# Performance work log

Measured on AMD Instinct MI355X. Metric: run time of the kernel, lower is better.

Reference implementation:

```python
import jax, jax.numpy as jnp
import numpy as np

EPS = 1e-5

def _bn_relu(y, mean, var, scale, bias):
    # y: (b, c, n); eval-mode batchnorm over channel axis, then ReLU
    inv = scale / jnp.sqrt(var + EPS)
    return jax.nn.relu((y - mean[None, :, None]) * inv[None, :, None] + bias[None, :, None])

def setup_inputs() -> dict:
    key = jax.random.key(0)
    ks = jax.random.split(key, 6)
    b, c, n, cr = 4, 256, 4096, 32
    inp = {
        'x': jax.random.normal(ks[0], (b, c, n), jnp.float32),
        'w_q': jax.random.normal(ks[1], (cr, c), jnp.float32) * (1.0 / np.sqrt(c)),
        'w_k': jax.random.normal(ks[2], (cr, c), jnp.float32) * (1.0 / np.sqrt(c)),
        'w_v': jax.random.normal(ks[3], (c, c), jnp.float32) * (1.0 / np.sqrt(c)),
        'bn1_scale': jnp.ones((cr,), jnp.float32), 'bn1_bias': jnp.zeros((cr,), jnp.float32),
        'bn1_mean': jnp.zeros((cr,), jnp.float32), 'bn1_var': jnp.ones((cr,), jnp.float32),
        'bn2_scale': jnp.ones((cr,), jnp.float32), 'bn2_bias': jnp.zeros((cr,), jnp.float32),
        'bn2_mean': jnp.zeros((cr,), jnp.float32), 'bn2_var': jnp.ones((cr,), jnp.float32),
        'bn3_scale': jnp.ones((c,), jnp.float32), 'bn3_bias': jnp.zeros((c,), jnp.float32),
        'bn3_mean': jnp.zeros((c,), jnp.float32), 'bn3_var': jnp.ones((c,), jnp.float32),
        'gamma': jax.random.normal(ks[4], (1,), jnp.float32),
    }
    return inp

def reference(x, w_q, w_k, w_v,
              bn1_scale, bn1_bias, bn1_mean, bn1_var,
              bn2_scale, bn2_bias, bn2_mean, bn2_var,
              bn3_scale, bn3_bias, bn3_mean, bn3_var,
              gamma):
    # x: (b, c, n). Original views as (b, c, n, 1) so width=1, height=n.
    b, c, n = x.shape
    # 1x1 conv == channel matmul, then BN+ReLU
    q = _bn_relu(jnp.einsum('oc,bcn->bon', w_q, x), bn1_mean, bn1_var, bn1_scale, bn1_bias)  # (b, c', n)
    k = _bn_relu(jnp.einsum('oc,bcn->bon', w_k, x), bn2_mean, bn2_var, bn2_scale, bn2_bias)  # (b, c', n)
    v = _bn_relu(jnp.einsum('oc,bcn->bon', w_v, x), bn3_mean, bn3_var, bn3_scale, bn3_bias)  # (b, c, n)
    # energy_H: (b, n, n) with -inf diagonal (self-attention along 'height')
    energy_h = jnp.einsum('bdi,bdj->bij', q, k)
    eye = jnp.eye(n, dtype=bool)
    energy_h = jnp.where(eye[None], -jnp.inf, energy_h)
    # energy_W: width=1 -> per-position self energy (b, n)
    energy_w = jnp.sum(q * k, axis=1)
    # softmax over concat of n H-logits and 1 W-logit
    att = jax.nn.softmax(jnp.concatenate([energy_h, energy_w[..., None]], axis=-1), axis=-1)  # (b, n, n+1)
    att_h = att[..., :n]        # (b, n, n), query i -> key j
    att_w = att[..., n]         # (b, n)
    out_h = jnp.einsum('bcj,bij->bci', v, att_h)   # aggregate values along height
    out_w = v * att_w[:, None, :]                  # width=1 self term
    out = gamma[0] * (out_h + out_w) + x
    return out
```

## Files before the change

### kernel.cpp

```cpp
#include <hip/hip_runtime.h>

#define Bb 4
#define Cc 256
#define Nn 4096
#define CR 32
#define EPS_BN 1e-5f
#define SHIFT2 28.853900817779268f
#define LOG2E  1.4426950408889634f
#define JSPLIT 4
#define JSL (Nn / JSPLIT)
#define TJ 64
#define NTILES (JSL / TJ)

typedef __attribute__((ext_vector_type(8))) short short8;
typedef __attribute__((ext_vector_type(4))) float f32x4;

__device__ inline unsigned int pk2(float a, float b) {
    __bf16 ha = (__bf16)a, hb = (__bf16)b;
    unsigned short ra = __builtin_bit_cast(unsigned short, ha);
    unsigned short rb = __builtin_bit_cast(unsigned short, hb);
    return ((unsigned int)rb << 16) | ra;
}
__device__ inline float blo(unsigned int u) { return __uint_as_float(u << 16); }
__device__ inline float bhi(unsigned int u) { return __uint_as_float(u & 0xffff0000u); }
__device__ inline float ex2(float x) { return __builtin_amdgcn_exp2f(x); }

__global__ __launch_bounds__(256) void qkv_kernel(
    const float* __restrict__ x,
    const float* __restrict__ wq, const float* __restrict__ wk, const float* __restrict__ wv,
    const float* __restrict__ bn1s, const float* __restrict__ bn1b, const float* __restrict__ bn1m, const float* __restrict__ bn1v,
    const float* __restrict__ bn2s, const float* __restrict__ bn2b, const float* __restrict__ bn2m, const float* __restrict__ bn2v,
    const float* __restrict__ bn3s, const float* __restrict__ bn3b, const float* __restrict__ bn3m, const float* __restrict__ bn3v,
    __bf16* __restrict__ Qt, __bf16* __restrict__ Kt, __bf16* __restrict__ Vb)
{
    __shared__ __align__(16) __bf16 F[16384];
    __shared__ __align__(16) float  sXf[4][32 * 40];
    __shared__ __align__(16) __bf16 sXt[4][2][32 * 40];

    const int tid = threadIdx.x;
    const int n0 = blockIdx.x * 128, g = blockIdx.y, b = blockIdx.z;
    const int lane = tid & 63, w = tid >> 6;
    const int l15 = lane & 15, l4 = lane >> 4;

    {
        int r = tid >> 2, q = tid & 3;
        int R = g * 64 + r;
        const float* src = (R < 32) ? (wq + (size_t)R * Cc)
                         : (R < 64) ? (wk + (size_t)(R - 32) * Cc)
                                    : (wv + (size_t)(R - 64) * Cc);
        int mt = r >> 4, l15r = r & 15;
#pragma unroll
        for (int u8 = 0; u8 < 8; ++u8) {
            float4 a = *(const float4*)&src[q * 64 + u8 * 8];
            float4 c2 = *(const float4*)&src[q * 64 + u8 * 8 + 4];
            uint4 p = { pk2(a.x,a.y), pk2(a.z,a.w), pk2(c2.x,c2.y), pk2(c2.z,c2.w) };
            int kc = 2 * q + (u8 >> 2), l4k = u8 & 3;
            *(uint4*)&F[(((kc * 4 + mt) * 64 + l4k * 16 + l15r)) * 8] = p;
        }
    }

    float*  sXfw  = &sXf[w][0];
    __bf16* sXtw0 = &sXt[w][0][0];
    __bf16* sXtw1 = &sXt[w][1][0];

    const int cr = lane >> 3, nq = lane & 7;
    const float* xbase = x + (size_t)(b * Cc + cr) * Nn + n0 + w * 32 + nq * 4;

    float4 xg[4];
#pragma unroll
    for (int it = 0; it < 4; ++it)
        xg[it] = *(const float4*)&xbase[(size_t)(it * 8) * Nn];

    __syncthreads();

    f32x4 acc[4][2];
#pragma unroll
    for (int mt = 0; mt < 4; ++mt)
#pragma unroll
        for (int nt = 0; nt < 2; ++nt) acc[mt][nt] = (f32x4){0.f, 0.f, 0.f, 0.f};

    for (int kc = 0; kc < 8; ++kc) {
#pragma unroll
        for (int it = 0; it < 4; ++it)
            *(float4*)&sXfw[(it * 8 + cr) * 40 + nq * 4] = xg[it];

        if (kc + 1 < 8) {
#pragma unroll
            for (int it = 0; it < 4; ++it)
                xg[it] = *(const float4*)&xbase[(size_t)((kc + 1) * 32 + it * 8) * Nn];
        }

#pragma unroll
        for (int s = 0; s < 2; ++s) {
            int n = lane & 31, c0 = (lane >> 5) * 8 + s * 16;
            float h[8], lo[8];
#pragma unroll
            for (int j = 0; j < 8; ++j) {
                float v = sXfw[(c0 + j) * 40 + n];
                float hh = (float)(__bf16)v;
                h[j] = hh; lo[j] = v - hh;
            }
            uint4 H = { pk2(h[0],h[1]), pk2(h[2],h[3]), pk2(h[4],h[5]), pk2(h[6],h[7]) };
            uint4 L = { pk2(lo[0],lo[1]), pk2(lo[2],lo[3]), pk2(lo[4],lo[5]), pk2(lo[6],lo[7]) };
            *(uint4*)&sXtw0[n * 40 + c0] = H;
            *(uint4*)&sXtw1[n * 40 + c0] = L;
        }

        short8 bh[2], bl[2];
#pragma unroll
        for (int nt = 0; nt < 2; ++nt) {
            bh[nt] = *(const short8*)&sXtw0[(nt * 16 + l15) * 40 + l4 * 8];
            bl[nt] = *(const short8*)&sXtw1[(nt * 16 + l15) * 40 + l4 * 8];
        }
#pragma unroll
        for (int mt = 0; mt < 4; ++mt) {
            short8 af = *(const short8*)&F[((kc * 4 + mt) * 64 + lane) * 8];
#pragma unroll
            for (int nt = 0; nt < 2; ++nt) {
                acc[mt][nt] = __builtin_amdgcn_mfma_f32_16x16x32_bf16(af, bh[nt], acc[mt][nt], 0, 0, 0);
                acc[mt][nt] = __builtin_amdgcn_mfma_f32_16x16x32_bf16(af, bl[nt], acc[mt][nt], 0, 0, 0);
            }
        }
    }

    if (g == 0) {
#pragma unroll
        for (int mt = 0; mt < 4; ++mt) {
            float scl[4], off[4];
#pragma unroll
            for (int r = 0; r < 4; ++r) {
                int R = mt * 16 + l4 * 4 + r;
                float s, o;
                if (R < 32) {
                    s = bn1s[R] * __frsqrt_rn(bn1v[R] + EPS_BN);
                    o = bn1b[R] - bn1m[R] * s;
                } else {
                    int row = R - 32;
                    s = bn2s[row] * __frsqrt_rn(bn2v[row] + EPS_BN);
                    o = bn2b[row] - bn2m[row] * s;
                    s *= LOG2E; o *= LOG2E;
                }
                scl[r] = s; off[r] = o;
            }
            __bf16* dst = (mt < 2) ? Qt : Kt;
            int d0 = (mt & 1) * 16 + l4 * 4;
#pragma unroll
            for (int nt = 0; nt < 2; ++nt) {
                f32x4 a = acc[mt][nt];
                float e0 = fmaxf(fmaf(a.x, scl[0], off[0]), 0.f);
                float e1 = fmaxf(fmaf(a.y, scl[1], off[1]), 0.f);
                float e2 = fmaxf(fmaf(a.z, scl[2], off[2]), 0.f);
                float e3 = fmaxf(fmaf(a.w, scl[3], off[3]), 0.f);
                uint2 p = { pk2(e0, e1), pk2(e2, e3) };
                int n = n0 + w * 32 + nt * 16 + l15;
                *(uint2*)&dst[(size_t)(b * Nn + n) * CR + d0] = p;
            }
        }
    } else {
        __bf16* oT = F;
        __syncthreads();
#pragma unroll
        for (int mt = 0; mt < 4; ++mt) {
            float scl[4], off[4];
#pragma unroll
            for (int r = 0; r < 4; ++r) {
                int row = (g - 1) * 64 + mt * 16 + l4 * 4 + r;
                float s = bn3s[row] * __frsqrt_rn(bn3v[row] + EPS_BN);
                scl[r] = s; off[r] = bn3b[row] - bn3m[row] * s;
            }
#pragma unroll
            for (int nt = 0; nt < 2; ++nt) {
                f32x4 a = acc[mt][nt];
                float e[4];
                e[0] = fmaxf(fmaf(a.x, scl[0], off[0]), 0.f);
                e[1] = fmaxf(fmaf(a.y, scl[1], off[1]), 0.f);
                e[2] = fmaxf(fmaf(a.z, scl[2], off[2]), 0.f);
                e[3] = fmaxf(fmaf(a.w, scl[3], off[3]), 0.f);
                int ncol = w * 32 + nt * 16 + l15;
#pragma unroll
                for (int r = 0; r < 4; ++r)
                    oT[(mt * 16 + l4 * 4 + r) * 136 + ncol] = (__bf16)e[r];
            }
        }
        __syncthreads();
        int rr = tid >> 2, qq = tid & 3;
        size_t vrow = (size_t)(b * Cc + (g - 1) * 64 + rr) * Nn + n0 + qq * 32;
#pragma unroll
        for (int e8 = 0; e8 < 4; ++e8)
            *(uint4*)&Vb[vrow + e8 * 8] = *(const uint4*)&oT[rr * 136 + qq * 32 + e8 * 8];
    }
}

__global__ __launch_bounds__(256) void attn_kernel(
    const __bf16* __restrict__ Qt, const __bf16* __restrict__ Kt,
    const __bf16* __restrict__ Vb,
    __bf16* __restrict__ PO, float* __restrict__ PL)
{
    __shared__ __align__(16) __bf16 sQ[64 * 40];
    __shared__ __align__(16) __bf16 sP[2][64 * 72];
    __shared__ __align__(16) float  sL[4][64];

    const int tid = threadIdx.x, lane = tid & 63, w = tid >> 6;
    const int b = blockIdx.z, js = blockIdx.y, iblk = blockIdx.x;
    const int i0 = iblk * 64;
    const int l15 = lane & 15, l4 = lane >> 4;

    {
        int i = tid >> 2, o = tid & 3;
        *(uint4*)&sQ[i * 40 + o * 8] =
            *(const uint4*)&Qt[(size_t)(b * Nn + i0 + i) * CR + o * 8];
    }
    __syncthreads();
    short8 qf[4];
#pragma unroll
    for (int it = 0; it < 4; ++it)
        qf[it] = *(const short8*)&sQ[(it * 16 + l15) * 40 + l4 * 8];

    f32x4 oacc[16];
#pragma unroll
    for (int z = 0; z < 16; ++z) oacc[z] = (f32x4){0.f, 0.f, 0.f, 0.f};
    float lp[4] = {0.f, 0.f, 0.f, 0.f};

    const size_t jb = (size_t)js * JSL;
    short8 kf = *(const short8*)&Kt[(size_t)(b * Nn + jb + 16 * w + l15) * CR + l4 * 8];

    for (int t = 0; t < NTILES; ++t) {
        const size_t j0 = jb + (size_t)t * TJ;
        __bf16* sPb = &sP[t & 1][0];

        short8 vf[8];
#pragma unroll
        for (int u = 0; u < 8; ++u) {
            int jh = u >> 2, ct = u & 3;
            int c = w * 64 + ct * 16 + l15;
            vf[u] = *(const short8*)&Vb[(size_t)(b * Cc + c) * Nn + j0 + (jh * 4 + l4) * 8];
        }

#pragma unroll
        for (int it = 0; it < 4; ++it) {
            f32x4 c0 = (f32x4){0.f, 0.f, 0.f, 0.f};
            c0 = __builtin_amdgcn_mfma_f32_16x16x32_bf16(kf, qf[it], c0, 0, 0, 0);
            float e0 = ex2(c0.x - SHIFT2);
            float e1 = ex2(c0.y - SHIFT2);
            float e2 = ex2(c0.z - SHIFT2);
            float e3 = ex2(c0.w - SHIFT2);
            lp[it] += (e0 + e1) + (e2 + e3);
            uint2 p2 = { pk2(e0, e1), pk2(e2, e3) };
            *(uint2*)&sP[t & 1][(it * 16 + l15) * 72 + w * 16 + l4 * 4] = p2;
        }
        __syncthreads();

        if (t + 1 < NTILES)
            kf = *(const short8*)&Kt[(size_t)(b * Nn + j0 + TJ + 16 * w + l15) * CR + l4 * 8];

        __builtin_amdgcn_s_setprio(1);
#pragma unroll
        for (int jh = 0; jh < 2; ++jh) {
            short8 pf[4];
#pragma unroll
            for (int it = 0; it < 4; ++it)
                pf[it] = *(const short8*)&sPb[(it * 16 + l15) * 72 + jh * 32 + l4 * 8];
#pragma unroll
            for (int ct = 0; ct < 4; ++ct) {
#pragma unroll
                for (int it = 0; it < 4; ++it)
                    oacc[it * 4 + ct] = __builtin_amdgcn_mfma_f32_16x16x32_bf16(
                        pf[it], vf[jh * 4 + ct], oacc[it * 4 + ct], 0, 0, 0);
            }
        }
        __builtin_amdgcn_s_setprio(0);
    }

#pragma unroll
    for (int it = 0; it < 4; ++it) {
        float v = lp[it];
        v += __shfl_xor(v, 16);
        v += __shfl_xor(v, 32);
        if (lane < 16) sL[w][it * 16 + lane] = v;
    }
    __syncthreads();
    if (tid < 64)
        PL[(size_t)(js * Bb + b) * Nn + i0 + tid] =
            sL[0][tid] + sL[1][tid] + sL[2][tid] + sL[3][tid];

    const size_t base = (size_t)((js * Bb + b) * (Nn / 64) + iblk) * 16384;
#pragma unroll
    for (int it = 0; it < 4; ++it)
#pragma unroll
        for (int ct = 0; ct < 4; ++ct) {
            f32x4 a = oacc[it * 4 + ct];
            uint2 p = { pk2(a.x, a.y), pk2(a.z, a.w) };
            *(uint2*)&PO[base + (size_t)((((w * 4 + it) * 4 + ct) * 64 + lane)) * 4] = p;
        }
}

__global__ __launch_bounds__(256) void reduce_kernel(
    const __bf16* __restrict__ PO, const float* __restrict__ PL,
    const float* __restrict__ x, const float* __restrict__ gamma,
    float* __restrict__ out)
{
    __shared__ __align__(16) float oT[64 * 68];
    __shared__ float sLinv[64];

    const int tid = threadIdx.x;
    const int iblk = blockIdx.x, wq = blockIdx.y, b = blockIdx.z;
    const int i0 = iblk * 64;
    const int lane = tid & 63, ct = tid >> 6, l15 = lane & 15, l4 = lane >> 4;

    if (tid < 64) {
        float l = 0.f;
#pragma unroll
        for (int js = 0; js < JSPLIT; ++js)
            l += PL[(size_t)(js * Bb + b) * Nn + i0 + tid];
        sLinv[tid] = 1.0f / l;
    }

    float o[4][4];
#pragma unroll
    for (int it = 0; it < 4; ++it) {
        o[it][0] = o[it][1] = o[it][2] = o[it][3] = 0.f;
#pragma unroll
        for (int js = 0; js < JSPLIT; ++js) {
            size_t base = (size_t)((js * Bb + b) * (Nn / 64) + iblk) * 16384;
            uint2 v = *(const uint2*)&PO[base + (size_t)((((wq * 4 + it) * 4 + ct) * 64 + lane)) * 4];
            o[it][0] += blo(v.x); o[it][1] += bhi(v.x);
            o[it][2] += blo(v.y); o[it][3] += bhi(v.y);
        }
    }

    const int cl = ct * 16 + l15;
#pragma unroll
    for (int it = 0; it < 4; ++it) {
        float4 t4 = { o[it][0], o[it][1], o[it][2], o[it][3] };
        *(float4*)&oT[cl * 68 + it * 16 + l4 * 4] = t4;
    }
    __syncthreads();

    const float g = gamma[0];
    const int c_l = tid >> 2, icol = (tid & 3) * 16;
    const int cg = wq * 64 + c_l;
    const size_t gb = (size_t)(b * Cc + cg) * Nn + i0 + icol;
#pragma unroll
    for (int k4 = 0; k4 < 4; ++k4) {
        float4 ov = *(const float4*)&oT[c_l * 68 + icol + k4 * 4];
        float4 li = *(const float4*)&sLinv[icol + k4 * 4];
        float4 xv = *(const float4*)&x[gb + k4 * 4];
        float4 res;
        res.x = fmaf(g, ov.x * li.x, xv.x);
        res.y = fmaf(g, ov.y * li.y, xv.y);
        res.z = fmaf(g, ov.z * li.z, xv.z);
        res.w = fmaf(g, ov.w * li.w, xv.w);
        *(float4*)&out[gb + k4 * 4] = res;
    }
}

extern "C" void kernel_launch(void* const* d_in, const int* in_sizes, int n_in,
                              void* d_out, int out_size, void* d_ws, size_t ws_size,
                              hipStream_t stream)
{
    const float* x    = (const float*)d_in[0];
    const float* wq   = (const float*)d_in[1];
    const float* wk   = (const float*)d_in[2];
    const float* wv   = (const float*)d_in[3];
    const float* bn1s = (const float*)d_in[4];
    const float* bn1b = (const float*)d_in[5];
    const float* bn1m = (const float*)d_in[6];
    const float* bn1v = (const float*)d_in[7];
    const float* bn2s = (const float*)d_in[8];
    const float* bn2b = (const float*)d_in[9];
    const float* bn2m = (const float*)d_in[10];
    const float* bn2v = (const float*)d_in[11];
    const float* bn3s = (const float*)d_in[12];
    const float* bn3b = (const float*)d_in[13];
    const float* bn3m = (const float*)d_in[14];
    const float* bn3v = (const float*)d_in[15];
    const float* gmm  = (const float*)d_in[16];
    float* out = (float*)d_out;

    char* ws = (char*)d_ws;
    __bf16* Qt  = (__bf16*)(ws);
    __bf16* Kt  = (__bf16*)(ws + (1u << 20));
    __bf16* Vb  = (__bf16*)(ws + (2u << 20));
    char*   big = ws + (10u << 20);
    __bf16* PO  = (__bf16*)big;
    float*  PL  = (float*)(big + 33554432);

    qkv_kernel<<<dim3(Nn / 128, 5, Bb), 256, 0, stream>>>(
        x, wq, wk, wv,
        bn1s, bn1b, bn1m, bn1v,
        bn2s, bn2b, bn2m, bn2v,
        bn3s, bn3b, bn3m, bn3v,
        Qt, Kt, Vb);

    attn_kernel<<<dim3(Nn / 64, JSPLIT, Bb), 256, 0, stream>>>(Qt, Kt, Vb, PO, PL);

    reduce_kernel<<<dim3(Nn / 64, 4, Bb), 256, 0, stream>>>(PO, PL, x, gmm, out);
}
```

Baseline: 213.9 us.

## Software-pipeline attention loop: compute next P tile and prefetch V during PV MFMA

```diff
diff --git a/kernel.cpp b/kernel.cpp
--- a/kernel.cpp
+++ b/kernel.cpp
@@ -191,7 +191,7 @@
     }
 }
 
-__global__ __launch_bounds__(256) void attn_kernel(
+__global__ __launch_bounds__(256, 4) void attn_kernel(
     const __bf16* __restrict__ Qt, const __bf16* __restrict__ Kt,
     const __bf16* __restrict__ Vb,
     __bf16* __restrict__ PO, float* __restrict__ PL)
@@ -222,36 +222,47 @@
     float lp[4] = {0.f, 0.f, 0.f, 0.f};
 
     const size_t jb = (size_t)js * JSL;
+
     short8 kf = *(const short8*)&Kt[(size_t)(b * Nn + jb + 16 * w + l15) * CR + l4 * 8];
+
+    short8 vf[8];
+#pragma unroll
+    for (int u = 0; u < 8; ++u) {
+        int jh = u >> 2, ct = u & 3;
+        int c = w * 64 + ct * 16 + l15;
+        vf[u] = *(const short8*)&Vb[(size_t)(b * Cc + c) * Nn + jb + (jh * 4 + l4) * 8];
+    }
+
+#pragma unroll
+    for (int it = 0; it < 4; ++it) {
+        f32x4 c0 = (f32x4){0.f, 0.f, 0.f, 0.f};
+        c0 = __builtin_amdgcn_mfma_f32_16x16x32_bf16(kf, qf[it], c0, 0, 0, 0);
+        float e0 = ex2(c0.x - SHIFT2), e1 = ex2(c0.y - SHIFT2);
+        float e2 = ex2(c0.z - SHIFT2), e3 = ex2(c0.w - SHIFT2);
+        lp[it] += (e0 + e1) + (e2 + e3);
+        uint2 p2 = { pk2(e0, e1), pk2(e2, e3) };
+        *(uint2*)&sP[0][(it * 16 + l15) * 72 + w * 16 + l4 * 4] = p2;
+    }
+    kf = *(const short8*)&Kt[(size_t)(b * Nn + jb + TJ + 16 * w + l15) * CR + l4 * 8];
+    __syncthreads();
 
     for (int t = 0; t < NTILES; ++t) {
         const size_t j0 = jb + (size_t)t * TJ;
-        __bf16* sPb = &sP[t & 1][0];
-
-        short8 vf[8];
-#pragma unroll
-        for (int u = 0; u < 8; ++u) {
-            int jh = u >> 2, ct = u & 3;
-            int c = w * 64 + ct * 16 + l15;
-            vf[u] = *(const short8*)&Vb[(size_t)(b * Cc + c) * Nn + j0 + (jh * 4 + l4) * 8];
-        }
-
-#pragma unroll
-        for (int it = 0; it < 4; ++it) {
-            f32x4 c0 = (f32x4){0.f, 0.f, 0.f, 0.f};
-            c0 = __builtin_amdgcn_mfma_f32_16x16x32_bf16(kf, qf[it], c0, 0, 0, 0);
-            float e0 = ex2(c0.x - SHIFT2);
-            float e1 = ex2(c0.y - SHIFT2);
-            float e2 = ex2(c0.z - SHIFT2);
-            float e3 = ex2(c0.w - SHIFT2);
-            lp[it] += (e0 + e1) + (e2 + e3);
-            uint2 p2 = { pk2(e0, e1), pk2(e2, e3) };
-            *(uint2*)&sP[t & 1][(it * 16 + l15) * 72 + w * 16 + l4 * 4] = p2;
-        }
-        __syncthreads();
-
-        if (t + 1 < NTILES)
-            kf = *(const short8*)&Kt[(size_t)(b * Nn + j0 + TJ + 16 * w + l15) * CR + l4 * 8];
+        const __bf16* sPr = &sP[t & 1][0];
+        __bf16*       sPn = &sP[(t + 1) & 1][0];
+
+        if (t + 1 < NTILES) {
+#pragma unroll
+            for (int it = 0; it < 4; ++it) {
+                f32x4 c0 = (f32x4){0.f, 0.f, 0.f, 0.f};
+                c0 = __builtin_amdgcn_mfma_f32_16x16x32_bf16(kf, qf[it], c0, 0, 0, 0);
+                float e0 = ex2(c0.x - SHIFT2), e1 = ex2(c0.y - SHIFT2);
+                float e2 = ex2(c0.z - SHIFT2), e3 = ex2(c0.w - SHIFT2);
+                lp[it] += (e0 + e1) + (e2 + e3);
+                uint2 p2 = { pk2(e0, e1), pk2(e2, e3) };
+                *(uint2*)&sPn[(it * 16 + l15) * 72 + w * 16 + l4 * 4] = p2;
+            }
+        }
 
         __builtin_amdgcn_s_setprio(1);
 #pragma unroll
@@ -259,7 +270,7 @@
             short8 pf[4];
 #pragma unroll
             for (int it = 0; it < 4; ++it)
-                pf[it] = *(const short8*)&sPb[(it * 16 + l15) * 72 + jh * 32 + l4 * 8];
+                pf[it] = *(const short8*)&sPr[(it * 16 + l15) * 72 + jh * 32 + l4 * 8];
 #pragma unroll
             for (int ct = 0; ct < 4; ++ct) {
 #pragma unroll
@@ -269,6 +280,18 @@
             }
         }
         __builtin_amdgcn_s_setprio(0);
+
+        if (t + 1 < NTILES) {
+#pragma unroll
+            for (int u = 0; u < 8; ++u) {
+                int jh = u >> 2, ct = u & 3;
+                int c = w * 64 + ct * 16 + l15;
+                vf[u] = *(const short8*)&Vb[(size_t)(b * Cc + c) * Nn + j0 + TJ + (jh * 4 + l4) * 8];
+            }
+            if (t + 2 < NTILES)
+                kf = *(const short8*)&Kt[(size_t)(b * Nn + j0 + 2 * TJ + 16 * w + l15) * CR + l4 * 8];
+            __syncthreads();
+        }
     }
 
 #pragma unroll
```

Measured after the change: 269.9 us. 1.26x slower.
